# Kernel tuning notes

Measured on AMD Instinct MI355X. Metric: run time of the kernel, lower is better.

## Reference

```python
import jax, jax.numpy as jnp
import numpy as np

B = 1_048_576
NUM_ITERS = 10  # training-mode default; eval mode uses 1000
EPS = 1e-12
LOW, HIGH = 0.02, 0.98  # SquashedSigmoid bounds


def setup_inputs() -> dict:
    key = jax.random.key(0)
    ks = jax.random.split(key, 4)
    # margins are population masses -> keep strictly positive
    margins = jax.random.uniform(ks[0], (B, 8), dtype=jnp.float32) + 0.1

    def lin(k, i, o):
        return (jax.random.normal(k, (i, o), jnp.float32) / np.sqrt(i)).astype(jnp.float32)

    return {
        "margins": margins,
        "W1": lin(ks[1], 8, 32), "b1": jnp.zeros((32,), jnp.float32),
        "W2": lin(ks[2], 32, 16), "b2": jnp.zeros((16,), jnp.float32),
        "W3": lin(ks[3], 16, 9), "b3": jnp.zeros((9,), jnp.float32),
    }


def tau_batched(p):
    # p: (B,4) positive params -> (B,3,3) positive couples matrix.
    # 2x2 core, extended by geometric-mean row/col (user-supplied tau in repo).
    a = p.reshape(-1, 2, 2)
    col3 = jnp.sqrt(a[:, :, 0] * a[:, :, 1])          # (B,2)
    row3 = jnp.sqrt(a[:, 0, :] * a[:, 1, :])          # (B,2)
    corner = jnp.sqrt(row3[:, 0] * row3[:, 1])        # (B,)
    top = jnp.concatenate([a, col3[:, :, None]], axis=2)                 # (B,2,3)
    bot = jnp.concatenate([row3, corner[:, None]], axis=1)[:, None, :]   # (B,1,3)
    return jnp.concatenate([top, bot], axis=1)        # (B,3,3)


def sinkhorn_knopp(A, row_margins, col_margins, iters):
    # Batched Sinkhorn-Knopp: A (B,R,C), row_margins (B,R), col_margins (B,C)
    r = row_margins[:, :, None]
    c = col_margins[:, None, :]

    def body(A, _):
        A = A * (r / (A.sum(axis=2, keepdims=True) + EPS))
        A = A * (c / (A.sum(axis=1, keepdims=True) + EPS))
        return A, None

    A, _ = jax.lax.scan(body, A, None, length=iters)
    return A


def reference(margins, W1, b1, W2, b2, W3, b3):
    Bn = margins.shape[0]
    M, F = margins[:, 0:3], margins[:, 3:6]

    # MLP: Linear-ReLU-Linear-ReLU-Linear
    h = jax.nn.relu(margins @ W1 + b1)
    h = jax.nn.relu(h @ W2 + b2)
    pars = h @ W3 + b3                                   # (B,9)

    muc = tau_batched(jnp.exp(pars[:, 0:4]))             # (B,3,3)
    sqs = lambda x: LOW + (HIGH - LOW) * jax.nn.sigmoid(x)
    shm, shf = sqs(pars[:, 4:6]), sqs(pars[:, 6:8])      # (B,2) each
    V = jnp.exp(pars[:, -1])                             # (B,)

    ones = jnp.ones((Bn, 1), margins.dtype)
    shm0 = jnp.concatenate([shm, ones], axis=1)          # (B,3)
    shf0 = jnp.concatenate([shf, ones], axis=1)          # (B,3)
    mucm0, muc0f = M * shm0, F * shf0                    # matched masses (margins)
    mum0, mu0f = M * (1.0 - shm0), F * (1.0 - shf0)      # singles

    muc = sinkhorn_knopp(muc, mucm0, muc0f, NUM_ITERS)   # (B,3,3)

    top = jnp.concatenate([muc, mum0[:, :, None]], axis=2)   # (B,3,4)
    bot = jnp.concatenate(
        [mu0f[:, None, :], jnp.zeros((Bn, 1, 1), margins.dtype)], axis=2)  # (B,1,4)
    mus = jnp.concatenate([top, bot], axis=1)            # (B,4,4)
    return mus, V
```

## Files before the change

kernel.cpp:

```cpp
#include <hip/hip_runtime.h>
#include <math.h>


#define QLOW  0.02f
#define QSPAN 0.96f
#define L2E   1.44269504088896f

constexpr int R = 2;

typedef __attribute__((ext_vector_type(2))) float f32x2;

__device__ __forceinline__ float frcp(float x) { return __builtin_amdgcn_rcpf(x); }
__device__ __forceinline__ f32x2 pfma(f32x2 a, f32x2 b, f32x2 c) {
    return __builtin_elementwise_fma(a, b, c);
}

__global__ __launch_bounds__(256) void sinkhorn_fused(
    const float* __restrict__ margins,
    const float* __restrict__ W1, const float* __restrict__ b1,
    const float* __restrict__ W2, const float* __restrict__ b2,
    const float* __restrict__ W3, const float* __restrict__ b3,
    float* __restrict__ out, int n)
{
    const int tid  = blockIdx.x * blockDim.x + threadIdx.x;
    const int lane = tid & 63;
    const int base = (tid >> 6) * (64 * R) + lane;

    const float4* __restrict__ m4 = (const float4*)margins;

    float m[R][8];
#pragma unroll
    for (int r = 0; r < R; ++r) {
        const int row = base + 64 * r;
        const float4 a0 = m4[row * 2 + 0];
        const float4 a1 = m4[row * 2 + 1];
        m[r][0] = a0.x; m[r][1] = a0.y; m[r][2] = a0.z; m[r][3] = a0.w;
        m[r][4] = a1.x; m[r][5] = a1.y; m[r][6] = a1.z; m[r][7] = a1.w;
    }

    const f32x2* __restrict__ W1v = (const f32x2*)W1;
    const f32x2* __restrict__ W2v = (const f32x2*)W2;
    const f32x2* __restrict__ b1v = (const f32x2*)b1;
    const f32x2* __restrict__ b2v = (const f32x2*)b2;

    f32x2 h1[R][16];
#pragma unroll
    for (int j = 0; j < 16; ++j) {
        const f32x2 bb = b1v[j];
#pragma unroll
        for (int r = 0; r < R; ++r) h1[r][j] = bb;
    }
#pragma unroll
    for (int k = 0; k < 8; ++k) {
        f32x2 mk[R];
#pragma unroll
        for (int r = 0; r < R; ++r) { mk[r].x = m[r][k]; mk[r].y = m[r][k]; }
#pragma unroll
        for (int j = 0; j < 16; ++j) {
            const f32x2 w = W1v[k * 16 + j];
#pragma unroll
            for (int r = 0; r < R; ++r) h1[r][j] = pfma(mk[r], w, h1[r][j]);
        }
    }
    const f32x2 zero2 = {0.0f, 0.0f};
#pragma unroll
    for (int j = 0; j < 16; ++j)
#pragma unroll
        for (int r = 0; r < R; ++r)
            h1[r][j] = __builtin_elementwise_max(h1[r][j], zero2);

    f32x2 h2[R][8];
#pragma unroll
    for (int j = 0; j < 8; ++j) {
        const f32x2 bb = b2v[j];
#pragma unroll
        for (int r = 0; r < R; ++r) h2[r][j] = bb;
    }
#pragma unroll
    for (int k = 0; k < 32; ++k) {
        f32x2 hk[R];
#pragma unroll
        for (int r = 0; r < R; ++r) {
            const float s = (k & 1) ? h1[r][k >> 1].y : h1[r][k >> 1].x;
            hk[r].x = s; hk[r].y = s;
        }
#pragma unroll
        for (int j = 0; j < 8; ++j) {
            const f32x2 w = W2v[k * 8 + j];
#pragma unroll
            for (int r = 0; r < R; ++r) h2[r][j] = pfma(hk[r], w, h2[r][j]);
        }
    }
#pragma unroll
    for (int j = 0; j < 8; ++j)
#pragma unroll
        for (int r = 0; r < R; ++r)
            h2[r][j] = __builtin_elementwise_max(h2[r][j], zero2);

    f32x2 p01[R], p23[R], p45[R], p67[R];
    float p8[R];
    {
        const f32x2 b01 = {b3[0], b3[1]};
        const f32x2 b23 = {b3[2], b3[3]};
        const f32x2 b45 = {b3[4], b3[5]};
        const f32x2 b67 = {b3[6], b3[7]};
        const float b8  = b3[8];
#pragma unroll
        for (int r = 0; r < R; ++r) {
            p01[r] = b01; p23[r] = b23; p45[r] = b45; p67[r] = b67; p8[r] = b8;
        }
    }
#pragma unroll
    for (int k = 0; k < 16; ++k) {
        const f32x2 w01 = {W3[k * 9 + 0], W3[k * 9 + 1]};
        const f32x2 w23 = {W3[k * 9 + 2], W3[k * 9 + 3]};
        const f32x2 w45 = {W3[k * 9 + 4], W3[k * 9 + 5]};
        const f32x2 w67 = {W3[k * 9 + 6], W3[k * 9 + 7]};
        const float w8  = W3[k * 9 + 8];
#pragma unroll
        for (int r = 0; r < R; ++r) {
            const float s = (k & 1) ? h2[r][k >> 1].y : h2[r][k >> 1].x;
            f32x2 hb; hb.x = s; hb.y = s;
            p01[r] = pfma(hb, w01, p01[r]);
            p23[r] = pfma(hb, w23, p23[r]);
            p45[r] = pfma(hb, w45, p45[r]);
            p67[r] = pfma(hb, w67, p67[r]);
            p8[r]  = fmaf(s, w8, p8[r]);
        }
    }

    float4* __restrict__ o4 = (float4*)out;
    float* __restrict__ oV = out + (size_t)n * 16;

#pragma unroll
    for (int r = 0; r < R; ++r) {
        const int row = base + 64 * r;

        const float l0 = p01[r].x * L2E, l1 = p01[r].y * L2E;
        const float l2 = p23[r].x * L2E, l3 = p23[r].y * L2E;

        const float a00 = exp2f(l0), a01 = exp2f(l1);
        const float a10 = exp2f(l2), a11 = exp2f(l3);
        const float h01 = (l0 + l1) * 0.5f, h23 = (l2 + l3) * 0.5f;
        const float a02 = exp2f(h01);
        const float a12 = exp2f(h23);
        const float a20 = exp2f((l0 + l2) * 0.5f);
        const float a21 = exp2f((l1 + l3) * 0.5f);
        const float a22 = exp2f((h01 + h23) * 0.5f);

        const float s4 = fmaf(QSPAN, frcp(1.0f + exp2f(-L2E * p45[r].x)), QLOW);
        const float s5 = fmaf(QSPAN, frcp(1.0f + exp2f(-L2E * p45[r].y)), QLOW);
        const float s6 = fmaf(QSPAN, frcp(1.0f + exp2f(-L2E * p67[r].x)), QLOW);
        const float s7 = fmaf(QSPAN, frcp(1.0f + exp2f(-L2E * p67[r].y)), QLOW);

        const float M0 = m[r][0], M1 = m[r][1], M2 = m[r][2];
        const float F0 = m[r][3], F1 = m[r][4], F2 = m[r][5];

        const float rm0 = M0 * s4, rm1 = M1 * s5, rm2 = M2;
        const float cm0 = F0 * s6, cm1 = F1 * s7, cm2 = F2;
        const float um0 = fmaf(-s4, M0, M0);
        const float um1 = fmaf(-s5, M1, M1);
        const float uf0 = fmaf(-s6, F0, F0);
        const float uf1 = fmaf(-s7, F1, F1);

        float v0 = 1.0f, v1 = 1.0f, v2 = 1.0f;
        float u0 = 1.0f, u1 = 1.0f, u2 = 1.0f;
#pragma unroll
        for (int it = 0; it < 10; ++it) {
            const float t0 = fmaf(a02, v2, fmaf(a01, v1, a00 * v0));
            const float t1 = fmaf(a12, v2, fmaf(a11, v1, a10 * v0));
            const float t2 = fmaf(a22, v2, fmaf(a21, v1, a20 * v0));
            u0 = rm0 * frcp(t0);
            u1 = rm1 * frcp(t1);
            u2 = rm2 * frcp(t2);
            const float q0 = fmaf(a20, u2, fmaf(a10, u1, a00 * u0));
            const float q1 = fmaf(a21, u2, fmaf(a11, u1, a01 * u0));
            const float q2 = fmaf(a22, u2, fmaf(a12, u1, a02 * u0));
            v0 = cm0 * frcp(q0);
            v1 = cm1 * frcp(q1);
            v2 = cm2 * frcp(q2);
        }

        o4[row * 4 + 0] = make_float4(u0 * a00 * v0, u0 * a01 * v1, u0 * a02 * v2, um0);
        o4[row * 4 + 1] = make_float4(u1 * a10 * v0, u1 * a11 * v1, u1 * a12 * v2, um1);
        o4[row * 4 + 2] = make_float4(u2 * a20 * v0, u2 * a21 * v1, u2 * a22 * v2, 0.0f);
        o4[row * 4 + 3] = make_float4(uf0, uf1, 0.0f, 0.0f);
        oV[row] = exp2f(p8[r] * L2E);
    }
}

extern "C" void kernel_launch(void* const* d_in, const int* in_sizes, int n_in,
                              void* d_out, int out_size, void* d_ws, size_t ws_size,
                              hipStream_t stream) {
    const float* margins = (const float*)d_in[0];
    const float* W1 = (const float*)d_in[1];
    const float* b1 = (const float*)d_in[2];
    const float* W2 = (const float*)d_in[3];
    const float* b2 = (const float*)d_in[4];
    const float* W3 = (const float*)d_in[5];
    const float* b3 = (const float*)d_in[6];

    const int n = in_sizes[0] / 8;
    const int threads = n / R;
    dim3 block(256), grid(threads / 256);

    sinkhorn_fused<<<grid, block, 0, stream>>>(margins, W1, b1, W2, b2, W3, b3,
                                               (float*)d_out, n);
}
```

Baseline: 128.0 us.

## Pack two rows across f32x2 lanes, stream MLP layers, prescale Sinkhorn matrices

Changes the packed-math layout so each f32x2 lane holds a different batch row, which lets the Sinkhorn iterations, exps and sigmoids run as packed ops as well. The first two MLP layers are fused by computing each hidden-1 unit and immediately accumulating it into hidden-2, so the 32-wide intermediate never has to be held in registers. The Sinkhorn loop is rewritten in scaled form: the margins are folded into precomputed B and C matrices, the first iteration starts from row sums, and the final column update is skipped, removing multiplies from the dependent chain. Weights are now read as scalars and broadcast rather than loaded as vector pairs, and the reformulation slightly changes the rounding order.

```diff
diff --git a/kernel.cpp b/kernel.cpp
--- a/kernel.cpp
+++ b/kernel.cpp
@@ -6,13 +6,24 @@
 #define QSPAN 0.96f
 #define L2E   1.44269504088896f
 
-constexpr int R = 2;
-
 typedef __attribute__((ext_vector_type(2))) float f32x2;
 
 __device__ __forceinline__ float frcp(float x) { return __builtin_amdgcn_rcpf(x); }
 __device__ __forceinline__ f32x2 pfma(f32x2 a, f32x2 b, f32x2 c) {
     return __builtin_elementwise_fma(a, b, c);
+}
+__device__ __forceinline__ f32x2 pmax0(f32x2 a) {
+    const f32x2 z = {0.0f, 0.0f};
+    return __builtin_elementwise_max(a, z);
+}
+__device__ __forceinline__ f32x2 prcp(f32x2 x) {
+    f32x2 r; r.x = frcp(x.x); r.y = frcp(x.y); return r;
+}
+__device__ __forceinline__ f32x2 pexp2(f32x2 x) {
+    f32x2 r; r.x = exp2f(x.x); r.y = exp2f(x.y); return r;
+}
+__device__ __forceinline__ f32x2 bc(float s) {
+    f32x2 r; r.x = s; r.y = s; return r;
 }
 
 __global__ __launch_bounds__(256) void sinkhorn_fused(
@@ -24,169 +35,127 @@
 {
     const int tid  = blockIdx.x * blockDim.x + threadIdx.x;
     const int lane = tid & 63;
-    const int base = (tid >> 6) * (64 * R) + lane;
+    const int base = (tid >> 6) * 128 + lane;
+    const int r0 = base, r1 = base + 64;
 
     const float4* __restrict__ m4 = (const float4*)margins;
+    const float4 a0A = m4[r0 * 2 + 0], a0B = m4[r0 * 2 + 1];
+    const float4 a1A = m4[r1 * 2 + 0], a1B = m4[r1 * 2 + 1];
 
-    float m[R][8];
-#pragma unroll
-    for (int r = 0; r < R; ++r) {
-        const int row = base + 64 * r;
-        const float4 a0 = m4[row * 2 + 0];
-        const float4 a1 = m4[row * 2 + 1];
-        m[r][0] = a0.x; m[r][1] = a0.y; m[r][2] = a0.z; m[r][3] = a0.w;
-        m[r][4] = a1.x; m[r][5] = a1.y; m[r][6] = a1.z; m[r][7] = a1.w;
-    }
+    f32x2 mp[8];
+    mp[0] = (f32x2){a0A.x, a1A.x}; mp[1] = (f32x2){a0A.y, a1A.y};
+    mp[2] = (f32x2){a0A.z, a1A.z}; mp[3] = (f32x2){a0A.w, a1A.w};
+    mp[4] = (f32x2){a0B.x, a1B.x}; mp[5] = (f32x2){a0B.y, a1B.y};
+    mp[6] = (f32x2){a0B.z, a1B.z}; mp[7] = (f32x2){a0B.w, a1B.w};
 
-    const f32x2* __restrict__ W1v = (const f32x2*)W1;
-    const f32x2* __restrict__ W2v = (const f32x2*)W2;
-    const f32x2* __restrict__ b1v = (const f32x2*)b1;
-    const f32x2* __restrict__ b2v = (const f32x2*)b2;
-
-    f32x2 h1[R][16];
-#pragma unroll
-    for (int j = 0; j < 16; ++j) {
-        const f32x2 bb = b1v[j];
-#pragma unroll
-        for (int r = 0; r < R; ++r) h1[r][j] = bb;
-    }
-#pragma unroll
-    for (int k = 0; k < 8; ++k) {
-        f32x2 mk[R];
-#pragma unroll
-        for (int r = 0; r < R; ++r) { mk[r].x = m[r][k]; mk[r].y = m[r][k]; }
-#pragma unroll
-        for (int j = 0; j < 16; ++j) {
-            const f32x2 w = W1v[k * 16 + j];
-#pragma unroll
-            for (int r = 0; r < R; ++r) h1[r][j] = pfma(mk[r], w, h1[r][j]);
-        }
-    }
-    const f32x2 zero2 = {0.0f, 0.0f};
-#pragma unroll
-    for (int j = 0; j < 16; ++j)
-#pragma unroll
-        for (int r = 0; r < R; ++r)
-            h1[r][j] = __builtin_elementwise_max(h1[r][j], zero2);
-
-    f32x2 h2[R][8];
-#pragma unroll
-    for (int j = 0; j < 8; ++j) {
-        const f32x2 bb = b2v[j];
-#pragma unroll
-        for (int r = 0; r < R; ++r) h2[r][j] = bb;
-    }
+    f32x2 h2p[16];
 #pragma unroll
     for (int k = 0; k < 32; ++k) {
-        f32x2 hk[R];
+        f32x2 h = mp[0] * bc(W1[k]);
 #pragma unroll
-        for (int r = 0; r < R; ++r) {
-            const float s = (k & 1) ? h1[r][k >> 1].y : h1[r][k >> 1].x;
-            hk[r].x = s; hk[r].y = s;
-        }
+        for (int kk = 1; kk < 8; ++kk)
+            h = pfma(mp[kk], bc(W1[kk * 32 + k]), h);
+        h = pmax0(h + bc(b1[k]));
+        if (k == 0) {
 #pragma unroll
-        for (int j = 0; j < 8; ++j) {
-            const f32x2 w = W2v[k * 8 + j];
+            for (int j = 0; j < 16; ++j) h2p[j] = h * bc(W2[j]);
+        } else {
 #pragma unroll
-            for (int r = 0; r < R; ++r) h2[r][j] = pfma(hk[r], w, h2[r][j]);
+            for (int j = 0; j < 16; ++j)
+                h2p[j] = pfma(h, bc(W2[k * 16 + j]), h2p[j]);
         }
     }
 #pragma unroll
-    for (int j = 0; j < 8; ++j)
+    for (int j = 0; j < 16; ++j) h2p[j] = pmax0(h2p[j] + bc(b2[j]));
+
+    f32x2 pp[9];
 #pragma unroll
-        for (int r = 0; r < R; ++r)
-            h2[r][j] = __builtin_elementwise_max(h2[r][j], zero2);
+    for (int j = 0; j < 9; ++j) pp[j] = h2p[0] * bc(W3[j]);
+#pragma unroll
+    for (int k = 1; k < 16; ++k)
+#pragma unroll
+        for (int j = 0; j < 9; ++j)
+            pp[j] = pfma(h2p[k], bc(W3[k * 9 + j]), pp[j]);
+#pragma unroll
+    for (int j = 0; j < 9; ++j) pp[j] = pp[j] + bc(b3[j]);
 
-    f32x2 p01[R], p23[R], p45[R], p67[R];
-    float p8[R];
-    {
-        const f32x2 b01 = {b3[0], b3[1]};
-        const f32x2 b23 = {b3[2], b3[3]};
-        const f32x2 b45 = {b3[4], b3[5]};
-        const f32x2 b67 = {b3[6], b3[7]};
-        const float b8  = b3[8];
+    const f32x2 l0 = pp[0] * bc(L2E), l1 = pp[1] * bc(L2E);
+    const f32x2 l2 = pp[2] * bc(L2E), l3 = pp[3] * bc(L2E);
+    const f32x2 a00 = pexp2(l0), a01 = pexp2(l1);
+    const f32x2 a10 = pexp2(l2), a11 = pexp2(l3);
+    const f32x2 h01 = (l0 + l1) * bc(0.5f), h23 = (l2 + l3) * bc(0.5f);
+    const f32x2 a02 = pexp2(h01);
+    const f32x2 a12 = pexp2(h23);
+    const f32x2 a20 = pexp2((l0 + l2) * bc(0.5f));
+    const f32x2 a21 = pexp2((l1 + l3) * bc(0.5f));
+    const f32x2 a22 = pexp2((h01 + h23) * bc(0.5f));
+
+    const f32x2 one2 = {1.0f, 1.0f};
+    const f32x2 s4 = pfma(bc(QSPAN), prcp(one2 + pexp2(pp[4] * bc(-L2E))), bc(QLOW));
+    const f32x2 s5 = pfma(bc(QSPAN), prcp(one2 + pexp2(pp[5] * bc(-L2E))), bc(QLOW));
+    const f32x2 s6 = pfma(bc(QSPAN), prcp(one2 + pexp2(pp[6] * bc(-L2E))), bc(QLOW));
+    const f32x2 s7 = pfma(bc(QSPAN), prcp(one2 + pexp2(pp[7] * bc(-L2E))), bc(QLOW));
+
+    const f32x2 M0 = mp[0], M1 = mp[1], M2 = mp[2];
+    const f32x2 F0 = mp[3], F1 = mp[4], F2 = mp[5];
+
+    const f32x2 rm0 = M0 * s4, rm1 = M1 * s5, rm2 = M2;
+    const f32x2 cm0 = F0 * s6, cm1 = F1 * s7, cm2 = F2;
+    const f32x2 um0 = pfma(-s4, M0, M0);
+    const f32x2 um1 = pfma(-s5, M1, M1);
+    const f32x2 uf0 = pfma(-s6, F0, F0);
+    const f32x2 uf1 = pfma(-s7, F1, F1);
+
+    const f32x2 B00 = a00 * rm0, B01 = a01 * rm0, B02 = a02 * rm0;
+    const f32x2 B10 = a10 * rm1, B11 = a11 * rm1, B12 = a12 * rm1;
+    const f32x2 B20 = a20 * rm2, B21 = a21 * rm2, B22 = a22 * rm2;
+    const f32x2 C00 = a00 * cm0, C01 = a01 * cm1, C02 = a02 * cm2;
+    const f32x2 C10 = a10 * cm0, C11 = a11 * cm1, C12 = a12 * cm2;
+    const f32x2 C20 = a20 * cm0, C21 = a21 * cm1, C22 = a22 * cm2;
+
+    f32x2 t0 = (a00 + a01) + a02;
+    f32x2 t1 = (a10 + a11) + a12;
+    f32x2 t2 = (a20 + a21) + a22;
+    f32x2 z0, z1, z2, w0, w1, w2;
 #pragma unroll
-        for (int r = 0; r < R; ++r) {
-            p01[r] = b01; p23[r] = b23; p45[r] = b45; p67[r] = b67; p8[r] = b8;
+    for (int it = 0; it < 10; ++it) {
+        z0 = prcp(t0); z1 = prcp(t1); z2 = prcp(t2);
+        const f32x2 q0 = pfma(B20, z2, pfma(B10, z1, B00 * z0));
+        const f32x2 q1 = pfma(B21, z2, pfma(B11, z1, B01 * z0));
+        const f32x2 q2 = pfma(B22, z2, pfma(B12, z1, B02 * z0));
+        w0 = prcp(q0); w1 = prcp(q1); w2 = prcp(q2);
+        if (it < 9) {
+            t0 = pfma(C02, w2, pfma(C01, w1, C00 * w0));
+            t1 = pfma(C12, w2, pfma(C11, w1, C10 * w0));
+            t2 = pfma(C22, w2, pfma(C21, w1, C20 * w0));
         }
     }
-#pragma unroll
-    for (int k = 0; k < 16; ++k) {
-        const f32x2 w01 = {W3[k * 9 + 0], W3[k * 9 + 1]};
-        const f32x2 w23 = {W3[k * 9 + 2], W3[k * 9 + 3]};
-        const f32x2 w45 = {W3[k * 9 + 4], W3[k * 9 + 5]};
-        const f32x2 w67 = {W3[k * 9 + 6], W3[k * 9 + 7]};
-        const float w8  = W3[k * 9 + 8];
-#pragma unroll
-        for (int r = 0; r < R; ++r) {
-            const float s = (k & 1) ? h2[r][k >> 1].y : h2[r][k >> 1].x;
-            f32x2 hb; hb.x = s; hb.y = s;
-            p01[r] = pfma(hb, w01, p01[r]);
-            p23[r] = pfma(hb, w23, p23[r]);
-            p45[r] = pfma(hb, w45, p45[r]);
-            p67[r] = pfma(hb, w67, p67[r]);
-            p8[r]  = fmaf(s, w8, p8[r]);
-        }
-    }
+    const f32x2 u0 = rm0 * z0, u1 = rm1 * z1, u2 = rm2 * z2;
+    const f32x2 v0 = cm0 * w0, v1 = cm1 * w1, v2 = cm2 * w2;
+
+    const f32x2 uv00 = u0 * v0, uv01 = u0 * v1, uv02 = u0 * v2;
+    const f32x2 uv10 = u1 * v0, uv11 = u1 * v1, uv12 = u1 * v2;
+    const f32x2 uv20 = u2 * v0, uv21 = u2 * v1, uv22 = u2 * v2;
+    const f32x2 A00 = uv00 * a00, A01 = uv01 * a01, A02 = uv02 * a02;
+    const f32x2 A10 = uv10 * a10, A11 = uv11 * a11, A12 = uv12 * a12;
+    const f32x2 A20 = uv20 * a20, A21 = uv21 * a21, A22 = uv22 * a22;
+
+    const f32x2 Vv = pexp2(pp[8] * bc(L2E));
 
     float4* __restrict__ o4 = (float4*)out;
     float* __restrict__ oV = out + (size_t)n * 16;
 
-#pragma unroll
-    for (int r = 0; r < R; ++r) {
-        const int row = base + 64 * r;
+    o4[r0 * 4 + 0] = make_float4(A00.x, A01.x, A02.x, um0.x);
+    o4[r0 * 4 + 1] = make_float4(A10.x, A11.x, A12.x, um1.x);
+    o4[r0 * 4 + 2] = make_float4(A20.x, A21.x, A22.x, 0.0f);
+    o4[r0 * 4 + 3] = make_float4(uf0.x, uf1.x, 0.0f, 0.0f);
+    oV[r0] = Vv.x;
 
-        const float l0 = p01[r].x * L2E, l1 = p01[r].y * L2E;
-        const float l2 = p23[r].x * L2E, l3 = p23[r].y * L2E;
-
-        const float a00 = exp2f(l0), a01 = exp2f(l1);
-        const float a10 = exp2f(l2), a11 = exp2f(l3);
-        const float h01 = (l0 + l1) * 0.5f, h23 = (l2 + l3) * 0.5f;
-        const float a02 = exp2f(h01);
-        const float a12 = exp2f(h23);
-        const float a20 = exp2f((l0 + l2) * 0.5f);
-        const float a21 = exp2f((l1 + l3) * 0.5f);
-        const float a22 = exp2f((h01 + h23) * 0.5f);
-
-        const float s4 = fmaf(QSPAN, frcp(1.0f + exp2f(-L2E * p45[r].x)), QLOW);
-        const float s5 = fmaf(QSPAN, frcp(1.0f + exp2f(-L2E * p45[r].y)), QLOW);
-        const float s6 = fmaf(QSPAN, frcp(1.0f + exp2f(-L2E * p67[r].x)), QLOW);
-        const float s7 = fmaf(QSPAN, frcp(1.0f + exp2f(-L2E * p67[r].y)), QLOW);
-
-        const float M0 = m[r][0], M1 = m[r][1], M2 = m[r][2];
-        const float F0 = m[r][3], F1 = m[r][4], F2 = m[r][5];
-
-        const float rm0 = M0 * s4, rm1 = M1 * s5, rm2 = M2;
-        const float cm0 = F0 * s6, cm1 = F1 * s7, cm2 = F2;
-        const float um0 = fmaf(-s4, M0, M0);
-        const float um1 = fmaf(-s5, M1, M1);
-        const float uf0 = fmaf(-s6, F0, F0);
-        const float uf1 = fmaf(-s7, F1, F1);
-
-        float v0 = 1.0f, v1 = 1.0f, v2 = 1.0f;
-        float u0 = 1.0f, u1 = 1.0f, u2 = 1.0f;
-#pragma unroll
-        for (int it = 0; it < 10; ++it) {
-            const float t0 = fmaf(a02, v2, fmaf(a01, v1, a00 * v0));
-            const float t1 = fmaf(a12, v2, fmaf(a11, v1, a10 * v0));
-            const float t2 = fmaf(a22, v2, fmaf(a21, v1, a20 * v0));
-            u0 = rm0 * frcp(t0);
-            u1 = rm1 * frcp(t1);
-            u2 = rm2 * frcp(t2);
-            const float q0 = fmaf(a20, u2, fmaf(a10, u1, a00 * u0));
-            const float q1 = fmaf(a21, u2, fmaf(a11, u1, a01 * u0));
-            const float q2 = fmaf(a22, u2, fmaf(a12, u1, a02 * u0));
-            v0 = cm0 * frcp(q0);
-            v1 = cm1 * frcp(q1);
-            v2 = cm2 * frcp(q2);
-        }
-
-        o4[row * 4 + 0] = make_float4(u0 * a00 * v0, u0 * a01 * v1, u0 * a02 * v2, um0);
-        o4[row * 4 + 1] = make_float4(u1 * a10 * v0, u1 * a11 * v1, u1 * a12 * v2, um1);
-        o4[row * 4 + 2] = make_float4(u2 * a20 * v0, u2 * a21 * v1, u2 * a22 * v2, 0.0f);
-        o4[row * 4 + 3] = make_float4(uf0, uf1, 0.0f, 0.0f);
-        oV[row] = exp2f(p8[r] * L2E);
-    }
+    o4[r1 * 4 + 0] = make_float4(A00.y, A01.y, A02.y, um0.y);
+    o4[r1 * 4 + 1] = make_float4(A10.y, A11.y, A12.y, um1.y);
+    o4[r1 * 4 + 2] = make_float4(A20.y, A21.y, A22.y, 0.0f);
+    o4[r1 * 4 + 3] = make_float4(uf0.y, uf1.y, 0.0f, 0.0f);
+    oV[r1] = Vv.y;
 }
 
 extern "C" void kernel_launch(void* const* d_in, const int* in_sizes, int n_in,
@@ -201,7 +170,7 @@
     const float* b3 = (const float*)d_in[6];
 
     const int n = in_sizes[0] / 8;
-    const int threads = n / R;
+    const int threads = n / 2;
     dim3 block(256), grid(threads / 256);
 
     sinkhorn_fused<<<grid, block, 0, stream>>>(margins, W1, b1, W2, b2, W3, b3,
```

Measured after the change: 231.1 us. +80.5%, slower.

## Stage MLP weights in LDS, fold margins into Sinkhorn matrices, interleave rows

Applied to the files above, without the earlier changes.

Each block copies the MLP weights and biases into shared memory, padding W3 rows to 12, so the layers read them with float4 LDS loads instead of per-element global or scalar loads. The Sinkhorn loop is rewritten algebraically: row and column margins are pre-multiplied into two 3x3 matrices, which removes the per-iteration margin multiplies. The two rows per thread are interleaved inside each iteration to expose more independent work. In exchange the kernel gains a __syncthreads, LDS traffic, extra live registers, and an occupancy hint of four blocks per SIMD/CU in the launch bounds.

```diff
diff --git a/kernel.cpp b/kernel.cpp
--- a/kernel.cpp
+++ b/kernel.cpp
@@ -15,13 +15,36 @@
     return __builtin_elementwise_fma(a, b, c);
 }
 
-__global__ __launch_bounds__(256) void sinkhorn_fused(
+__global__ __launch_bounds__(256, 4) void sinkhorn_fused(
     const float* __restrict__ margins,
     const float* __restrict__ W1, const float* __restrict__ b1,
     const float* __restrict__ W2, const float* __restrict__ b2,
     const float* __restrict__ W3, const float* __restrict__ b3,
     float* __restrict__ out, int n)
 {
+    __shared__ __align__(16) float sW1[256];
+    __shared__ __align__(16) float sW2[512];
+    __shared__ __align__(16) float sW3[16 * 12];
+    __shared__ __align__(16) float sB1[32];
+    __shared__ __align__(16) float sB2[16];
+    __shared__ __align__(16) float sB3[12];
+
+    {
+        const int t = threadIdx.x;
+        sW1[t] = W1[t];
+        sW2[t] = W2[t];
+        sW2[t + 256] = W2[t + 256];
+        if (t < 144) { const int k = t / 9, j = t - 9 * k; sW3[k * 12 + j] = W3[t]; }
+        if (t < 32) sB1[t] = b1[t];
+        if (t < 16) sB2[t] = b2[t];
+        if (t < 9)  sB3[t] = b3[t];
+    }
+    __syncthreads();
+
+    const float4* __restrict__ sW1q = (const float4*)sW1;
+    const float4* __restrict__ sW2q = (const float4*)sW2;
+    const float4* __restrict__ sW3q = (const float4*)sW3;
+
     const int tid  = blockIdx.x * blockDim.x + threadIdx.x;
     const int lane = tid & 63;
     const int base = (tid >> 6) * (64 * R) + lane;
@@ -38,15 +61,10 @@
         m[r][4] = a1.x; m[r][5] = a1.y; m[r][6] = a1.z; m[r][7] = a1.w;
     }
 
-    const f32x2* __restrict__ W1v = (const f32x2*)W1;
-    const f32x2* __restrict__ W2v = (const f32x2*)W2;
-    const f32x2* __restrict__ b1v = (const f32x2*)b1;
-    const f32x2* __restrict__ b2v = (const f32x2*)b2;
-
     f32x2 h1[R][16];
 #pragma unroll
     for (int j = 0; j < 16; ++j) {
-        const f32x2 bb = b1v[j];
+        const f32x2 bb = {sB1[2 * j], sB1[2 * j + 1]};
 #pragma unroll
         for (int r = 0; r < R; ++r) h1[r][j] = bb;
     }
@@ -56,10 +74,15 @@
 #pragma unroll
         for (int r = 0; r < R; ++r) { mk[r].x = m[r][k]; mk[r].y = m[r][k]; }
 #pragma unroll
-        for (int j = 0; j < 16; ++j) {
-            const f32x2 w = W1v[k * 16 + j];
-#pragma unroll
-            for (int r = 0; r < R; ++r) h1[r][j] = pfma(mk[r], w, h1[r][j]);
+        for (int j4 = 0; j4 < 8; ++j4) {
+            const float4 w = sW1q[k * 8 + j4];
+            const f32x2 wa = {w.x, w.y};
+            const f32x2 wb = {w.z, w.w};
+#pragma unroll
+            for (int r = 0; r < R; ++r) {
+                h1[r][2 * j4 + 0] = pfma(mk[r], wa, h1[r][2 * j4 + 0]);
+                h1[r][2 * j4 + 1] = pfma(mk[r], wb, h1[r][2 * j4 + 1]);
+            }
         }
     }
     const f32x2 zero2 = {0.0f, 0.0f};
@@ -72,7 +95,7 @@
     f32x2 h2[R][8];
 #pragma unroll
     for (int j = 0; j < 8; ++j) {
-        const f32x2 bb = b2v[j];
+        const f32x2 bb = {sB2[2 * j], sB2[2 * j + 1]};
 #pragma unroll
         for (int r = 0; r < R; ++r) h2[r][j] = bb;
     }
@@ -85,10 +108,15 @@
             hk[r].x = s; hk[r].y = s;
         }
 #pragma unroll
-        for (int j = 0; j < 8; ++j) {
-            const f32x2 w = W2v[k * 8 + j];
-#pragma unroll
-            for (int r = 0; r < R; ++r) h2[r][j] = pfma(hk[r], w, h2[r][j]);
+        for (int j4 = 0; j4 < 4; ++j4) {
+            const float4 w = sW2q[k * 4 + j4];
+            const f32x2 wa = {w.x, w.y};
+            const f32x2 wb = {w.z, w.w};
+#pragma unroll
+            for (int r = 0; r < R; ++r) {
+                h2[r][2 * j4 + 0] = pfma(hk[r], wa, h2[r][2 * j4 + 0]);
+                h2[r][2 * j4 + 1] = pfma(hk[r], wb, h2[r][2 * j4 + 1]);
+            }
         }
     }
 #pragma unroll
@@ -100,11 +128,11 @@
     f32x2 p01[R], p23[R], p45[R], p67[R];
     float p8[R];
     {
-        const f32x2 b01 = {b3[0], b3[1]};
-        const f32x2 b23 = {b3[2], b3[3]};
-        const f32x2 b45 = {b3[4], b3[5]};
-        const f32x2 b67 = {b3[6], b3[7]};
-        const float b8  = b3[8];
+        const f32x2 b01 = {sB3[0], sB3[1]};
+        const f32x2 b23 = {sB3[2], sB3[3]};
+        const f32x2 b45 = {sB3[4], sB3[5]};
+        const f32x2 b67 = {sB3[6], sB3[7]};
+        const float b8  = sB3[8];
 #pragma unroll
         for (int r = 0; r < R; ++r) {
             p01[r] = b01; p23[r] = b23; p45[r] = b45; p67[r] = b67; p8[r] = b8;
@@ -112,11 +140,13 @@
     }
 #pragma unroll
     for (int k = 0; k < 16; ++k) {
-        const f32x2 w01 = {W3[k * 9 + 0], W3[k * 9 + 1]};
-        const f32x2 w23 = {W3[k * 9 + 2], W3[k * 9 + 3]};
-        const f32x2 w45 = {W3[k * 9 + 4], W3[k * 9 + 5]};
-        const f32x2 w67 = {W3[k * 9 + 6], W3[k * 9 + 7]};
-        const float w8  = W3[k * 9 + 8];
+        const float4 wA = sW3q[k * 3 + 0];
+        const float4 wB = sW3q[k * 3 + 1];
+        const float w8  = sW3[k * 12 + 8];
+        const f32x2 w01 = {wA.x, wA.y};
+        const f32x2 w23 = {wA.z, wA.w};
+        const f32x2 w45 = {wB.x, wB.y};
+        const f32x2 w67 = {wB.z, wB.w};
 #pragma unroll
         for (int r = 0; r < R; ++r) {
             const float s = (k & 1) ? h2[r][k >> 1].y : h2[r][k >> 1].x;
@@ -129,13 +159,14 @@
         }
     }
 
-    float4* __restrict__ o4 = (float4*)out;
-    float* __restrict__ oV = out + (size_t)n * 16;
+    float Bm[R][9], Cm[R][9];
+    float t0_[R], t1_[R], t2_[R];
+    float rm_[R][3];
+    float um_[R][2], uf_[R][2];
+    float Vv[R];
 
 #pragma unroll
     for (int r = 0; r < R; ++r) {
-        const int row = base + 64 * r;
-
         const float l0 = p01[r].x * L2E, l1 = p01[r].y * L2E;
         const float l2 = p23[r].x * L2E, l3 = p23[r].y * L2E;
 
@@ -158,34 +189,74 @@
 
         const float rm0 = M0 * s4, rm1 = M1 * s5, rm2 = M2;
         const float cm0 = F0 * s6, cm1 = F1 * s7, cm2 = F2;
-        const float um0 = fmaf(-s4, M0, M0);
-        const float um1 = fmaf(-s5, M1, M1);
-        const float uf0 = fmaf(-s6, F0, F0);
-        const float uf1 = fmaf(-s7, F1, F1);
-
-        float v0 = 1.0f, v1 = 1.0f, v2 = 1.0f;
-        float u0 = 1.0f, u1 = 1.0f, u2 = 1.0f;
-#pragma unroll
-        for (int it = 0; it < 10; ++it) {
-            const float t0 = fmaf(a02, v2, fmaf(a01, v1, a00 * v0));
-            const float t1 = fmaf(a12, v2, fmaf(a11, v1, a10 * v0));
-            const float t2 = fmaf(a22, v2, fmaf(a21, v1, a20 * v0));
-            u0 = rm0 * frcp(t0);
-            u1 = rm1 * frcp(t1);
-            u2 = rm2 * frcp(t2);
-            const float q0 = fmaf(a20, u2, fmaf(a10, u1, a00 * u0));
-            const float q1 = fmaf(a21, u2, fmaf(a11, u1, a01 * u0));
-            const float q2 = fmaf(a22, u2, fmaf(a12, u1, a02 * u0));
-            v0 = cm0 * frcp(q0);
-            v1 = cm1 * frcp(q1);
-            v2 = cm2 * frcp(q2);
-        }
-
-        o4[row * 4 + 0] = make_float4(u0 * a00 * v0, u0 * a01 * v1, u0 * a02 * v2, um0);
-        o4[row * 4 + 1] = make_float4(u1 * a10 * v0, u1 * a11 * v1, u1 * a12 * v2, um1);
-        o4[row * 4 + 2] = make_float4(u2 * a20 * v0, u2 * a21 * v1, u2 * a22 * v2, 0.0f);
-        o4[row * 4 + 3] = make_float4(uf0, uf1, 0.0f, 0.0f);
-        oV[row] = exp2f(p8[r] * L2E);
+        rm_[r][0] = rm0; rm_[r][1] = rm1; rm_[r][2] = rm2;
+        um_[r][0] = fmaf(-s4, M0, M0);
+        um_[r][1] = fmaf(-s5, M1, M1);
+        uf_[r][0] = fmaf(-s6, F0, F0);
+        uf_[r][1] = fmaf(-s7, F1, F1);
+
+        Bm[r][0] = a00 * rm0; Bm[r][1] = a01 * rm0; Bm[r][2] = a02 * rm0;
+        Bm[r][3] = a10 * rm1; Bm[r][4] = a11 * rm1; Bm[r][5] = a12 * rm1;
+        Bm[r][6] = a20 * rm2; Bm[r][7] = a21 * rm2; Bm[r][8] = a22 * rm2;
+        Cm[r][0] = a00 * cm0; Cm[r][1] = a01 * cm1; Cm[r][2] = a02 * cm2;
+        Cm[r][3] = a10 * cm0; Cm[r][4] = a11 * cm1; Cm[r][5] = a12 * cm2;
+        Cm[r][6] = a20 * cm0; Cm[r][7] = a21 * cm1; Cm[r][8] = a22 * cm2;
+
+        t0_[r] = (a00 + a01) + a02;
+        t1_[r] = (a10 + a11) + a12;
+        t2_[r] = (a20 + a21) + a22;
+
+        Vv[r] = exp2f(p8[r] * L2E);
+    }
+
+    float z0_[R], z1_[R], z2_[R], w0_[R], w1_[R], w2_[R];
+#pragma unroll
+    for (int it = 0; it < 10; ++it) {
+#pragma unroll
+        for (int r = 0; r < R; ++r) {
+            z0_[r] = frcp(t0_[r]);
+            z1_[r] = frcp(t1_[r]);
+            z2_[r] = frcp(t2_[r]);
+        }
+#pragma unroll
+        for (int r = 0; r < R; ++r) {
+            const float q0 = fmaf(Bm[r][6], z2_[r], fmaf(Bm[r][3], z1_[r], Bm[r][0] * z0_[r]));
+            const float q1 = fmaf(Bm[r][7], z2_[r], fmaf(Bm[r][4], z1_[r], Bm[r][1] * z0_[r]));
+            const float q2 = fmaf(Bm[r][8], z2_[r], fmaf(Bm[r][5], z1_[r], Bm[r][2] * z0_[r]));
+            w0_[r] = frcp(q0);
+            w1_[r] = frcp(q1);
+            w2_[r] = frcp(q2);
+        }
+        if (it < 9) {
+#pragma unroll
+            for (int r = 0; r < R; ++r) {
+                t0_[r] = fmaf(Cm[r][2], w2_[r], fmaf(Cm[r][1], w1_[r], Cm[r][0] * w0_[r]));
+                t1_[r] = fmaf(Cm[r][5], w2_[r], fmaf(Cm[r][4], w1_[r], Cm[r][3] * w0_[r]));
+                t2_[r] = fmaf(Cm[r][8], w2_[r], fmaf(Cm[r][7], w1_[r], Cm[r][6] * w0_[r]));
+            }
+        }
+    }
+
+    float4* __restrict__ o4 = (float4*)out;
+    float* __restrict__ oV = out + (size_t)n * 16;
+
+#pragma unroll
+    for (int r = 0; r < R; ++r) {
+        const int row = base + 64 * r;
+        const float u0 = rm_[r][0] * z0_[r];
+        const float u1 = rm_[r][1] * z1_[r];
+        const float u2 = rm_[r][2] * z2_[r];
+        const float w0 = w0_[r], w1 = w1_[r], w2 = w2_[r];
+
+        const float A0f = u0 * Cm[r][0] * w0, A1f = u0 * Cm[r][1] * w1, A2f = u0 * Cm[r][2] * w2;
+        const float A3f = u1 * Cm[r][3] * w0, A4f = u1 * Cm[r][4] * w1, A5f = u1 * Cm[r][5] * w2;
+        const float A6f = u2 * Cm[r][6] * w0, A7f = u2 * Cm[r][7] * w1, A8f = u2 * Cm[r][8] * w2;
+
+        o4[row * 4 + 0] = make_float4(A0f, A1f, A2f, um_[r][0]);
+        o4[row * 4 + 1] = make_float4(A3f, A4f, A5f, um_[r][1]);
+        o4[row * 4 + 2] = make_float4(A6f, A7f, A8f, 0.0f);
+        o4[row * 4 + 3] = make_float4(uf_[r][0], uf_[r][1], 0.0f, 0.0f);
+        oV[row] = Vv[r];
     }
 }
 
```

After: 140.8 us. 10.0% more time.
